# Performance work log

Hardware: AMD Instinct MI355X
Metric: run time of the kernel (lower is better)

## Reference

```python
import jax, jax.numpy as jnp
import numpy as np

N = 50000     # nodes
E = 600000    # directed edges (avg degree 12)
F_IN = 128    # num_features
H = 128       # hidden_units
C = 16        # num_classes
G = 500       # graphs in batch


def setup_inputs() -> dict:
    key = jax.random.key(0)
    ks = jax.random.split(key, 6)
    x = jax.random.normal(ks[0], (N, F_IN), jnp.float32)
    edge_src = jax.random.randint(ks[1], (E,), 0, N, jnp.int32)
    edge_dst = jax.random.randint(ks[2], (E,), 0, N, jnp.int32)
    batch = jnp.sort(jax.random.randint(ks[3], (N,), 0, G, jnp.int32))
    W1 = jax.random.normal(ks[4], (F_IN, H), jnp.float32) / np.float32(np.sqrt(F_IN))
    b1 = jnp.zeros((H,), jnp.float32)
    W2 = jax.random.normal(ks[5], (H, C), jnp.float32) / np.float32(np.sqrt(H))
    b2 = jnp.zeros((C,), jnp.float32)
    return {"x": x, "W1": W1, "b1": b1, "W2": W2, "b2": b2,
            "edge_src": edge_src, "edge_dst": edge_dst, "batch": batch}


def _gcn_conv(x, W, b, src, dst, norm):
    # linear transform then normalized scatter-add aggregation (PyG GCNConv)
    h = x @ W                                   # [N, out]
    msg = h[src] * norm[:, None]                # [E+N, out]
    return jax.ops.segment_sum(msg, dst, num_segments=N) + b


def reference(x, W1, b1, W2, b2, edge_src, edge_dst, batch):
    # add self-loops
    loops = jnp.arange(N, dtype=edge_src.dtype)
    src = jnp.concatenate([edge_src, loops])
    dst = jnp.concatenate([edge_dst, loops])
    # symmetric normalization D^-1/2 A D^-1/2 (in-degree at targets)
    deg = jax.ops.segment_sum(jnp.ones_like(dst, jnp.float32), dst, num_segments=N)
    dis = jax.lax.rsqrt(deg)  # deg >= 1 because of self-loops
    norm = dis[src] * dis[dst]

    h = jax.nn.relu(_gcn_conv(x, W1, b1, src, dst, norm))
    h = _gcn_conv(h, W2, b2, src, dst, norm)

    # scatter_mean pooling over graphs
    counts = jax.ops.segment_sum(jnp.ones((N,), jnp.float32), batch, num_segments=G)
    pooled = jax.ops.segment_sum(h, batch, num_segments=G) / jnp.maximum(counts, 1.0)[:, None]
    return jax.nn.log_softmax(pooled, axis=1)
```

## Files before the change

### kernel.cpp

```cpp
#include <hip/hip_runtime.h>
#include <hip/hip_bf16.h>


#define NN 50000
#define EE 600000
#define FIN 128
#define HH 128
#define CC 16
#define GG 500
#define ETOT (EE + NN)
#define SBLK 196

typedef unsigned short ushort_t;
typedef unsigned int uint_t;

typedef __attribute__((ext_vector_type(8))) short bf16x8;
typedef __attribute__((ext_vector_type(8))) ushort_t u16x8;
typedef __attribute__((ext_vector_type(4))) ushort_t u16x4;
typedef __attribute__((ext_vector_type(4))) float f32x4;
typedef __attribute__((ext_vector_type(2))) float f32x2;

__device__ inline ushort_t f2bf(float f) {
    uint_t u = __float_as_uint(f);
    u = (u + 0x7FFFu + ((u >> 16) & 1u)) >> 16;
    return (ushort_t)u;
}
__device__ inline float bf2f(ushort_t b) {
    return __uint_as_float(((uint_t)b) << 16);
}

__global__ void init_kernel(int* cnt, float* pooled) {
    int i = blockIdx.x * blockDim.x + threadIdx.x;
    if (i < NN) cnt[i] = 0;
    if (i < GG * CC) pooled[i] = 0.0f;
}

__global__ void count_kernel(const int* __restrict__ edge_dst,
                             int* __restrict__ cnt, int* __restrict__ seq) {
    int idx = blockIdx.x * blockDim.x + threadIdx.x;
    if (idx < EE) seq[idx] = atomicAdd(&cnt[edge_dst[idx]], 1);
}

__device__ inline int block_excl_scan(int v, int t, int* total) {
    __shared__ int wsum[4];
    int lane = t & 63, wv = t >> 6;
    int inc = v;
    for (int off = 1; off < 64; off <<= 1) {
        int n = __shfl_up(inc, off);
        if (lane >= off) inc += n;
    }
    if (lane == 63) wsum[wv] = inc;
    __syncthreads();
    int off_w = 0;
    for (int w = 0; w < wv; w++) off_w += wsum[w];
    *total = wsum[0] + wsum[1] + wsum[2] + wsum[3];
    return off_w + inc - v;
}

__global__ __launch_bounds__(256) void scanA_kernel(const int* __restrict__ cnt,
                                                    int* __restrict__ rowptr,
                                                    float* __restrict__ dis,
                                                    int* __restrict__ bsum) {
    int t = threadIdx.x;
    int i = blockIdx.x * 256 + t;
    int d = 0;
    if (i < NN) {
        d = cnt[i] + 1;
        dis[i] = rsqrtf((float)d);
    }
    int total;
    int excl = block_excl_scan(d, t, &total);
    if (i < NN) rowptr[i] = excl;
    if (t == 0) bsum[blockIdx.x] = total;
}

__global__ __launch_bounds__(256) void scanB_kernel(const int* __restrict__ bsum,
                                                    int* __restrict__ boff,
                                                    int* __restrict__ rowptr) {
    int t = threadIdx.x;
    int v = (t < SBLK) ? bsum[t] : 0;
    int total;
    int excl = block_excl_scan(v, t, &total);
    if (t < SBLK) boff[t] = excl;
    if (t == 0) rowptr[NN] = total;
}

__global__ __launch_bounds__(256) void scanC_kernel(int* __restrict__ rowptr,
                                                    const int* __restrict__ boff) {
    int i = blockIdx.x * 256 + threadIdx.x;
    if (i < NN) rowptr[i] += boff[blockIdx.x];
}

__global__ void fill_kernel(const int* __restrict__ edge_src,
                            const int* __restrict__ edge_dst,
                            const float* __restrict__ dis,
                            const int* __restrict__ rowptr,
                            const int* __restrict__ seq,
                            int2* __restrict__ csr) {
    int idx = blockIdx.x * blockDim.x + threadIdx.x;
    if (idx < EE) {
        int s = edge_src[idx], d = edge_dst[idx];
        int pos = rowptr[d] + seq[idx];
        csr[pos] = make_int2(s, __float_as_int(dis[s] * dis[d]));
    } else if (idx < ETOT) {
        int n = idx - EE;
        float dn = dis[n];
        csr[rowptr[n + 1] - 1] = make_int2(n, __float_as_int(dn * dn));
    }
}

__global__ __launch_bounds__(256) void gemm1_kernel(const float* __restrict__ x,
                                                    const float* __restrict__ W1,
                                                    unsigned char* __restrict__ hb8) {
    __shared__ ushort_t xs[64 * 136];
    __shared__ ushort_t wt[128 * 136];
    int t = threadIdx.x;
    int row0 = blockIdx.x * 64;
    for (int i = 0; i < 8; i++) {
        int slot = t + i * 256;
        int r = slot >> 5, k4 = slot & 31;
        int gr = row0 + r;
        float4 v = (gr < NN) ? ((const float4*)x)[gr * 32 + k4]
                             : make_float4(0.f, 0.f, 0.f, 0.f);
        u16x4 bv = { f2bf(v.x), f2bf(v.y), f2bf(v.z), f2bf(v.w) };
        *(u16x4*)(&xs[r * 136 + k4 * 4]) = bv;
    }
    for (int i = 0; i < 16; i++) {
        int slot = t + i * 256;
        int k = slot >> 5, c4 = slot & 31;
        float4 v = ((const float4*)W1)[k * 32 + c4];
        wt[(c4 * 4 + 0) * 136 + k] = f2bf(v.x);
        wt[(c4 * 4 + 1) * 136 + k] = f2bf(v.y);
        wt[(c4 * 4 + 2) * 136 + k] = f2bf(v.z);
        wt[(c4 * 4 + 3) * 136 + k] = f2bf(v.w);
    }
    __syncthreads();

    int wave = t >> 6, lane = t & 63;
    int m = lane & 15, quad = lane >> 4;
    f32x4 acc[8];
    for (int ct = 0; ct < 8; ct++) acc[ct] = (f32x4)(0.0f);

    for (int ko = 0; ko < 4; ko++) {
        bf16x8 a = *(const bf16x8*)(&xs[(16 * wave + m) * 136 + ko * 32 + quad * 8]);
        for (int ct = 0; ct < 8; ct++) {
            bf16x8 b = *(const bf16x8*)(&wt[(ct * 16 + m) * 136 + ko * 32 + quad * 8]);
            acc[ct] = __builtin_amdgcn_mfma_f32_16x16x32_bf16(a, b, acc[ct], 0, 0, 0);
        }
    }
    for (int ct = 0; ct < 8; ct++) {
        int gcol = ct * 16 + m;
        for (int r = 0; r < 4; r++) {
            int grow = row0 + wave * 16 + quad * 4 + r;
            if (grow < NN) {
                int p = __builtin_amdgcn_cvt_pk_fp8_f32(acc[ct][r], 0.0f, 0, false);
                hb8[(size_t)grow * HH + gcol] = (unsigned char)(p & 0xFF);
            }
        }
    }
}

__global__ __launch_bounds__(256) void agg1_kernel(const unsigned char* __restrict__ hb8,
                                                   const int* __restrict__ rowptr,
                                                   const int2* __restrict__ csr,
                                                   const float* __restrict__ b1,
                                                   ushort_t* __restrict__ h1b) {
    int wave = threadIdx.x >> 6, lane = threadIdx.x & 63;
    int node = blockIdx.x * 4 + wave;
    if (node >= NN) return;
    int slot = lane >> 3, sub = lane & 7;
    int e0 = rowptr[node], e1 = rowptr[node + 1];
    float acc[16];
    for (int j = 0; j < 16; j++) acc[j] = 0.0f;
    for (int e = e0 + slot; e < e1; e += 8) {
        int2 ent = csr[e];
        float w = __int_as_float(ent.y);
        uint4 hv = *(const uint4*)(hb8 + (size_t)ent.x * HH + sub * 16);
        uint_t words[4] = { hv.x, hv.y, hv.z, hv.w };
        for (int q = 0; q < 4; q++) {
            f32x2 lo = __builtin_amdgcn_cvt_pk_f32_fp8(words[q], false);
            f32x2 hi = __builtin_amdgcn_cvt_pk_f32_fp8(words[q], true);
            acc[q * 4 + 0] += w * lo[0];
            acc[q * 4 + 1] += w * lo[1];
            acc[q * 4 + 2] += w * hi[0];
            acc[q * 4 + 3] += w * hi[1];
        }
    }
    for (int j = 0; j < 16; j++) {
        acc[j] += __shfl_xor(acc[j], 8);
        acc[j] += __shfl_xor(acc[j], 16);
        acc[j] += __shfl_xor(acc[j], 32);
    }
    if (slot == 0) {
        u16x8 o0, o1;
        for (int j = 0; j < 8; j++) {
            o0[j] = f2bf(fmaxf(acc[j]     + b1[sub * 16 + j],     0.0f));
            o1[j] = f2bf(fmaxf(acc[8 + j] + b1[sub * 16 + 8 + j], 0.0f));
        }
        *(u16x8*)(h1b + (size_t)node * HH + sub * 16)     = o0;
        *(u16x8*)(h1b + (size_t)node * HH + sub * 16 + 8) = o1;
    }
}

__global__ __launch_bounds__(256) void gemm2_kernel(const ushort_t* __restrict__ h1b,
                                                    const float* __restrict__ W2,
                                                    float* __restrict__ h2) {
    __shared__ ushort_t w2s[HH * CC];
    int t = threadIdx.x;
    for (int i = t; i < HH * CC; i += 256) w2s[i] = f2bf(W2[i]);
    __syncthreads();
    int wave = t >> 6, lane = t & 63;
    int m = lane & 15, quad = lane >> 4;
    int node0 = (blockIdx.x * 4 + wave) * 16;
    f32x4 acc = (f32x4)(0.0f);
    int arow = node0 + m;
    for (int ko = 0; ko < 4; ko++) {
        bf16x8 a = (bf16x8)(short)0;
        if (arow < NN)
            a = *(const bf16x8*)(h1b + (size_t)arow * HH + ko * 32 + quad * 8);
        bf16x8 b;
        for (int j = 0; j < 8; j++)
            b[j] = (short)w2s[(ko * 32 + quad * 8 + j) * CC + m];
        acc = __builtin_amdgcn_mfma_f32_16x16x32_bf16(a, b, acc, 0, 0, 0);
    }
    for (int r = 0; r < 4; r++) {
        int grow = node0 + quad * 4 + r;
        if (grow < NN) h2[grow * CC + m] = acc[r];
    }
}

__global__ __launch_bounds__(256) void agg2pool_kernel(const float* __restrict__ h2,
                                                       const int* __restrict__ rowptr,
                                                       const int2* __restrict__ csr,
                                                       const float* __restrict__ b2,
                                                       const int* __restrict__ batch,
                                                       float* __restrict__ pooled) {
    __shared__ float vals[16][16];
    __shared__ int gid[16];
    int t = threadIdx.x;
    int local = t >> 4, c = t & 15;
    int node = blockIdx.x * 16 + local;
    int e0 = rowptr[node], e1 = rowptr[node + 1];
    float acc = 0.0f;
    for (int e = e0; e < e1; e++) {
        int2 ent = csr[e];
        acc += __int_as_float(ent.y) * h2[(size_t)ent.x * CC + c];
    }
    vals[local][c] = acc + b2[c];
    if (c == 0) gid[local] = batch[node];
    __syncthreads();
    if (t < 16) {
        float run = 0.0f;
        for (int i = 0; i < 16; i++) {
            run += vals[i][t];
            if (i == 15 || gid[i + 1] != gid[i]) {
                atomicAdd(&pooled[gid[i] * CC + t], run);
                run = 0.0f;
            }
        }
    }
}

__global__ void lsm_kernel(const float* __restrict__ pooled,
                           const int* __restrict__ batch,
                           float* __restrict__ out) {
    int idx = blockIdx.x * blockDim.x + threadIdx.x;
    int g = idx >> 4, c = idx & 15;
    if (g >= GG) return;
    int lo = 0, hi = NN;
    while (lo < hi) { int mid = (lo + hi) >> 1; if (batch[mid] < g) lo = mid + 1; else hi = mid; }
    int lo2 = lo, hi2 = NN;
    while (lo2 < hi2) { int mid = (lo2 + hi2) >> 1; if (batch[mid] < g + 1) lo2 = mid + 1; else hi2 = mid; }
    float cnt = (float)(lo2 - lo);
    float v = pooled[g * CC + c] / fmaxf(cnt, 1.0f);
    float m = v;
    for (int off = 8; off >= 1; off >>= 1) m = fmaxf(m, __shfl_xor(m, off, 16));
    float s = expf(v - m);
    for (int off = 8; off >= 1; off >>= 1) s += __shfl_xor(s, off, 16);
    out[g * CC + c] = v - m - logf(s);
}

extern "C" void kernel_launch(void* const* d_in, const int* in_sizes, int n_in,
                              void* d_out, int out_size, void* d_ws, size_t ws_size,
                              hipStream_t stream) {
    const float* x  = (const float*)d_in[0];
    const float* W1 = (const float*)d_in[1];
    const float* b1 = (const float*)d_in[2];
    const float* W2 = (const float*)d_in[3];
    const float* b2 = (const float*)d_in[4];
    const int* edge_src = (const int*)d_in[5];
    const int* edge_dst = (const int*)d_in[6];
    const int* batch    = (const int*)d_in[7];
    float* out = (float*)d_out;

    char* ws = (char*)d_ws;
    size_t off = 0;
    auto alloc = [&](size_t bytes) {
        void* p = ws + off;
        off += (bytes + 255) & ~size_t(255);
        return p;
    };
    int*   cnt     = (int*)  alloc(NN * 4);
    float* dis     = (float*)alloc(NN * 4);
    int*   rowptr  = (int*)  alloc((NN + 1) * 4);
    int*   seq     = (int*)  alloc(EE * 4);
    int*   bsum    = (int*)  alloc(SBLK * 4);
    int*   boff    = (int*)  alloc(SBLK * 4);
    int2*  csr     = (int2*) alloc((size_t)ETOT * 8);
    unsigned char* hb8 = (unsigned char*)alloc((size_t)NN * HH);
    ushort_t* h1b  = (ushort_t*)alloc((size_t)NN * HH * 2);
    float* h2      = (float*)alloc((size_t)NN * CC * 4);
    float* pooled  = (float*)alloc(GG * CC * 4);

    const int B = 256;
    init_kernel<<<(NN + B - 1) / B, B, 0, stream>>>(cnt, pooled);
    count_kernel<<<(EE + B - 1) / B, B, 0, stream>>>(edge_dst, cnt, seq);
    scanA_kernel<<<SBLK, B, 0, stream>>>(cnt, rowptr, dis, bsum);
    scanB_kernel<<<1, B, 0, stream>>>(bsum, boff, rowptr);
    scanC_kernel<<<SBLK, B, 0, stream>>>(rowptr, boff);
    fill_kernel<<<(ETOT + B - 1) / B, B, 0, stream>>>(edge_src, edge_dst, dis,
                                                      rowptr, seq, csr);
    gemm1_kernel<<<(NN + 63) / 64, B, 0, stream>>>(x, W1, hb8);
    agg1_kernel<<<(NN + 3) / 4, B, 0, stream>>>(hb8, rowptr, csr, b1, h1b);
    gemm2_kernel<<<(NN + 63) / 64, B, 0, stream>>>(h1b, W2, h2);
    agg2pool_kernel<<<NN / 16, B, 0, stream>>>(h2, rowptr, csr, b2, batch, pooled);
    lsm_kernel<<<(GG * CC + B - 1) / B, B, 0, stream>>>(pooled, batch, out);
}
```

Before: 217.3 us.

## Factor GCN normalization into node-side scaling and shrink CSR to source-only indices

Splits the symmetric edge weight dis[s]*dis[d] into a source-side scale applied in the GEMM epilogues and a destination-side scale applied after aggregation. The CSR can then hold only 4-byte source indices, and the aggregation loops become pure adds. It also stores layer-2 features as bf16 instead of fp32 and merges the two scan-finalize kernels into one launch by hardcoding rowptr[NN]=ETOT. The goal is less memory traffic in the gather-heavy aggregation kernels and fewer launches, at the cost of some extra bf16/fp8 rounding of the pre-scaled features.

```diff
diff --git a/kernel.cpp b/kernel.cpp
--- a/kernel.cpp
+++ b/kernel.cpp
@@ -74,43 +74,39 @@
     if (t == 0) bsum[blockIdx.x] = total;
 }
 
-__global__ __launch_bounds__(256) void scanB_kernel(const int* __restrict__ bsum,
-                                                    int* __restrict__ boff,
-                                                    int* __restrict__ rowptr) {
+__global__ __launch_bounds__(256) void scanBC_kernel(int* __restrict__ rowptr,
+                                                     const int* __restrict__ bsum) {
+    __shared__ int sb[256];
     int t = threadIdx.x;
     int v = (t < SBLK) ? bsum[t] : 0;
     int total;
-    int excl = block_excl_scan(v, t, &total);
-    if (t < SBLK) boff[t] = excl;
-    if (t == 0) rowptr[NN] = total;
-}
-
-__global__ __launch_bounds__(256) void scanC_kernel(int* __restrict__ rowptr,
-                                                    const int* __restrict__ boff) {
-    int i = blockIdx.x * 256 + threadIdx.x;
-    if (i < NN) rowptr[i] += boff[blockIdx.x];
+    int ex = block_excl_scan(v, t, &total);
+    sb[t] = ex;
+    __syncthreads();
+    int myoff = sb[blockIdx.x];
+    int i = blockIdx.x * 256 + t;
+    if (i < NN) rowptr[i] += myoff;
+    if (blockIdx.x == 0 && t == 0) rowptr[NN] = ETOT;
 }
 
 __global__ void fill_kernel(const int* __restrict__ edge_src,
                             const int* __restrict__ edge_dst,
-                            const float* __restrict__ dis,
                             const int* __restrict__ rowptr,
                             const int* __restrict__ seq,
-                            int2* __restrict__ csr) {
+                            int* __restrict__ csr) {
     int idx = blockIdx.x * blockDim.x + threadIdx.x;
     if (idx < EE) {
-        int s = edge_src[idx], d = edge_dst[idx];
-        int pos = rowptr[d] + seq[idx];
-        csr[pos] = make_int2(s, __float_as_int(dis[s] * dis[d]));
+        int d = edge_dst[idx];
+        csr[rowptr[d] + seq[idx]] = edge_src[idx];
     } else if (idx < ETOT) {
         int n = idx - EE;
-        float dn = dis[n];
-        csr[rowptr[n + 1] - 1] = make_int2(n, __float_as_int(dn * dn));
+        csr[rowptr[n + 1] - 1] = n;
     }
 }
 
 __global__ __launch_bounds__(256) void gemm1_kernel(const float* __restrict__ x,
                                                     const float* __restrict__ W1,
+                                                    const float* __restrict__ dis,
                                                     unsigned char* __restrict__ hb8) {
     __shared__ ushort_t xs[64 * 136];
     __shared__ ushort_t wt[128 * 136];
@@ -148,12 +144,17 @@
             acc[ct] = __builtin_amdgcn_mfma_f32_16x16x32_bf16(a, b, acc[ct], 0, 0, 0);
         }
     }
+    float dsc[4];
+    for (int r = 0; r < 4; r++) {
+        int grow = row0 + wave * 16 + quad * 4 + r;
+        dsc[r] = (grow < NN) ? dis[grow] : 0.0f;
+    }
     for (int ct = 0; ct < 8; ct++) {
         int gcol = ct * 16 + m;
         for (int r = 0; r < 4; r++) {
             int grow = row0 + wave * 16 + quad * 4 + r;
             if (grow < NN) {
-                int p = __builtin_amdgcn_cvt_pk_fp8_f32(acc[ct][r], 0.0f, 0, false);
+                int p = __builtin_amdgcn_cvt_pk_fp8_f32(acc[ct][r] * dsc[r], 0.0f, 0, false);
                 hb8[(size_t)grow * HH + gcol] = (unsigned char)(p & 0xFF);
             }
         }
@@ -162,7 +163,8 @@
 
 __global__ __launch_bounds__(256) void agg1_kernel(const unsigned char* __restrict__ hb8,
                                                    const int* __restrict__ rowptr,
-                                                   const int2* __restrict__ csr,
+                                                   const int* __restrict__ csr,
+                                                   const float* __restrict__ dis,
                                                    const float* __restrict__ b1,
                                                    ushort_t* __restrict__ h1b) {
     int wave = threadIdx.x >> 6, lane = threadIdx.x & 63;
@@ -173,17 +175,16 @@
     float acc[16];
     for (int j = 0; j < 16; j++) acc[j] = 0.0f;
     for (int e = e0 + slot; e < e1; e += 8) {
-        int2 ent = csr[e];
-        float w = __int_as_float(ent.y);
-        uint4 hv = *(const uint4*)(hb8 + (size_t)ent.x * HH + sub * 16);
+        int s = csr[e];
+        uint4 hv = *(const uint4*)(hb8 + (size_t)s * HH + sub * 16);
         uint_t words[4] = { hv.x, hv.y, hv.z, hv.w };
         for (int q = 0; q < 4; q++) {
             f32x2 lo = __builtin_amdgcn_cvt_pk_f32_fp8(words[q], false);
             f32x2 hi = __builtin_amdgcn_cvt_pk_f32_fp8(words[q], true);
-            acc[q * 4 + 0] += w * lo[0];
-            acc[q * 4 + 1] += w * lo[1];
-            acc[q * 4 + 2] += w * hi[0];
-            acc[q * 4 + 3] += w * hi[1];
+            acc[q * 4 + 0] += lo[0];
+            acc[q * 4 + 1] += lo[1];
+            acc[q * 4 + 2] += hi[0];
+            acc[q * 4 + 3] += hi[1];
         }
     }
     for (int j = 0; j < 16; j++) {
@@ -192,10 +193,11 @@
         acc[j] += __shfl_xor(acc[j], 32);
     }
     if (slot == 0) {
+        float dn = dis[node];
         u16x8 o0, o1;
         for (int j = 0; j < 8; j++) {
-            o0[j] = f2bf(fmaxf(acc[j]     + b1[sub * 16 + j],     0.0f));
-            o1[j] = f2bf(fmaxf(acc[8 + j] + b1[sub * 16 + 8 + j], 0.0f));
+            o0[j] = f2bf(fmaxf(acc[j]     * dn + b1[sub * 16 + j],     0.0f));
+            o1[j] = f2bf(fmaxf(acc[8 + j] * dn + b1[sub * 16 + 8 + j], 0.0f));
         }
         *(u16x8*)(h1b + (size_t)node * HH + sub * 16)     = o0;
         *(u16x8*)(h1b + (size_t)node * HH + sub * 16 + 8) = o1;
@@ -204,7 +206,8 @@
 
 __global__ __launch_bounds__(256) void gemm2_kernel(const ushort_t* __restrict__ h1b,
                                                     const float* __restrict__ W2,
-                                                    float* __restrict__ h2) {
+                                                    const float* __restrict__ dis,
+                                                    ushort_t* __restrict__ h2b) {
     __shared__ ushort_t w2s[HH * CC];
     int t = threadIdx.x;
     for (int i = t; i < HH * CC; i += 256) w2s[i] = f2bf(W2[i]);
@@ -225,13 +228,14 @@
     }
     for (int r = 0; r < 4; r++) {
         int grow = node0 + quad * 4 + r;
-        if (grow < NN) h2[grow * CC + m] = acc[r];
-    }
-}
-
-__global__ __launch_bounds__(256) void agg2pool_kernel(const float* __restrict__ h2,
+        if (grow < NN) h2b[grow * CC + m] = f2bf(acc[r] * dis[grow]);
+    }
+}
+
+__global__ __launch_bounds__(256) void agg2pool_kernel(const ushort_t* __restrict__ h2b,
                                                        const int* __restrict__ rowptr,
-                                                       const int2* __restrict__ csr,
+                                                       const int* __restrict__ csr,
+                                                       const float* __restrict__ dis,
                                                        const float* __restrict__ b2,
                                                        const int* __restrict__ batch,
                                                        float* __restrict__ pooled) {
@@ -243,10 +247,9 @@
     int e0 = rowptr[node], e1 = rowptr[node + 1];
     float acc = 0.0f;
     for (int e = e0; e < e1; e++) {
-        int2 ent = csr[e];
-        acc += __int_as_float(ent.y) * h2[(size_t)ent.x * CC + c];
-    }
-    vals[local][c] = acc + b2[c];
+        acc += bf2f(h2b[(size_t)csr[e] * CC + c]);
+    }
+    vals[local][c] = acc * dis[node] + b2[c];
     if (c == 0) gid[local] = batch[node];
     __syncthreads();
     if (t < 16) {
@@ -305,24 +308,21 @@
     int*   rowptr  = (int*)  alloc((NN + 1) * 4);
     int*   seq     = (int*)  alloc(EE * 4);
     int*   bsum    = (int*)  alloc(SBLK * 4);
-    int*   boff    = (int*)  alloc(SBLK * 4);
-    int2*  csr     = (int2*) alloc((size_t)ETOT * 8);
+    int*   csr     = (int*)  alloc((size_t)ETOT * 4);
     unsigned char* hb8 = (unsigned char*)alloc((size_t)NN * HH);
     ushort_t* h1b  = (ushort_t*)alloc((size_t)NN * HH * 2);
-    float* h2      = (float*)alloc((size_t)NN * CC * 4);
+    ushort_t* h2b  = (ushort_t*)alloc((size_t)NN * CC * 2);
     float* pooled  = (float*)alloc(GG * CC * 4);
 
     const int B = 256;
     init_kernel<<<(NN + B - 1) / B, B, 0, stream>>>(cnt, pooled);
     count_kernel<<<(EE + B - 1) / B, B, 0, stream>>>(edge_dst, cnt, seq);
     scanA_kernel<<<SBLK, B, 0, stream>>>(cnt, rowptr, dis, bsum);
-    scanB_kernel<<<1, B, 0, stream>>>(bsum, boff, rowptr);
-    scanC_kernel<<<SBLK, B, 0, stream>>>(rowptr, boff);
-    fill_kernel<<<(ETOT + B - 1) / B, B, 0, stream>>>(edge_src, edge_dst, dis,
-                                                      rowptr, seq, csr);
-    gemm1_kernel<<<(NN + 63) / 64, B, 0, stream>>>(x, W1, hb8);
-    agg1_kernel<<<(NN + 3) / 4, B, 0, stream>>>(hb8, rowptr, csr, b1, h1b);
-    gemm2_kernel<<<(NN + 63) / 64, B, 0, stream>>>(h1b, W2, h2);
-    agg2pool_kernel<<<NN / 16, B, 0, stream>>>(h2, rowptr, csr, b2, batch, pooled);
+    scanBC_kernel<<<SBLK, B, 0, stream>>>(rowptr, bsum);
+    fill_kernel<<<(ETOT + B - 1) / B, B, 0, stream>>>(edge_src, edge_dst, rowptr, seq, csr);
+    gemm1_kernel<<<(NN + 63) / 64, B, 0, stream>>>(x, W1, dis, hb8);
+    agg1_kernel<<<(NN + 3) / 4, B, 0, stream>>>(hb8, rowptr, csr, dis, b1, h1b);
+    gemm2_kernel<<<(NN + 63) / 64, B, 0, stream>>>(h1b, W2, dis, h2b);
+    agg2pool_kernel<<<NN / 16, B, 0, stream>>>(h2b, rowptr, csr, dis, b2, batch, pooled);
     lsm_kernel<<<(GG * CC + B - 1) / B, B, 0, stream>>>(pooled, batch, out);
 }
```

Result: faster. 211.4 us (-2.7%).
